# Optimization experiments

Measured on AMD Instinct MI355X. Metric: run time of the kernel, lower is better.

## Reference

```python
import jax, jax.numpy as jnp
import numpy as np

B, N, S, C1, C2 = 8, 8192, 2048, 128, 256
IN_CH = C1 + C2
MLP = [256, 128]
EPS_INTERP = 1e-8
EPS_BN = 1e-5


def setup_inputs() -> dict:
    key = jax.random.key(0)
    ks = jax.random.split(key, 8)
    inp = {
        "xyz1": jax.random.normal(ks[0], (B, 3, N), dtype=jnp.float32),
        "xyz2": jax.random.normal(ks[1], (B, 3, S), dtype=jnp.float32),
        "points1": jax.random.normal(ks[2], (B, C1, N), dtype=jnp.float32),
        "points2": jax.random.normal(ks[3], (B, C2, S), dtype=jnp.float32),
        # Conv1d(k=1) weights as [out, in] matrices, plus BN gamma/beta
        "W1": jax.random.normal(ks[4], (MLP[0], IN_CH), dtype=jnp.float32) * 0.02,
        "b1": jnp.zeros((MLP[0],), dtype=jnp.float32),
        "g1": jnp.ones((MLP[0],), dtype=jnp.float32),
        "be1": jnp.zeros((MLP[0],), dtype=jnp.float32),
        "W2": jax.random.normal(ks[5], (MLP[1], MLP[0]), dtype=jnp.float32) * 0.02,
        "b2": jnp.zeros((MLP[1],), dtype=jnp.float32),
        "g2": jnp.ones((MLP[1],), dtype=jnp.float32),
        "be2": jnp.zeros((MLP[1],), dtype=jnp.float32),
    }
    return inp


def _conv_bn_relu(x, W, b, g, be):
    # x: [B, N, Cin]; 1x1 Conv1d == per-point matmul; BN over (batch, length) per channel (training-mode stats)
    y = jnp.einsum('bnc,oc->bno', x, W) + b
    m = jnp.mean(y, axis=(0, 1))
    v = jnp.var(y, axis=(0, 1))
    return jax.nn.relu((y - m) * jax.lax.rsqrt(v + EPS_BN) * g + be)


def reference(xyz1, xyz2, points1, points2, W1, b1, g1, be1, W2, b2, g2, be2):
    x1 = xyz1.transpose(0, 2, 1)   # [B, N, 3]
    x2 = xyz2.transpose(0, 2, 1)   # [B, S, 3]
    p2 = points2.transpose(0, 2, 1)  # [B, S, C2]
    p1 = points1.transpose(0, 2, 1)  # [B, N, C1]

    # squared pairwise distances [B, N, S]
    d = (jnp.sum(x1 * x1, axis=-1, keepdims=True)
         - 2.0 * jnp.einsum('bnd,bsd->bns', x1, x2)
         + jnp.sum(x2 * x2, axis=-1)[:, None, :])

    # 3 nearest neighbors (smallest distances)
    neg_d, idx = jax.lax.top_k(-d, 3)          # idx: [B, N, 3]
    d3 = -neg_d                                 # [B, N, 3]
    recip = 1.0 / (d3 + EPS_INTERP)
    w = recip / jnp.sum(recip, axis=-1, keepdims=True)  # [B, N, 3]

    gathered = jax.vmap(lambda p, i: p[i])(p2, idx)     # [B, N, 3, C2]
    interp = jnp.sum(gathered * w[..., None], axis=2)   # [B, N, C2]

    x = jnp.concatenate([p1, interp], axis=-1)          # [B, N, C1+C2]
    x = _conv_bn_relu(x, W1, b1, g1, be1)
    x = _conv_bn_relu(x, W2, b2, g2, be2)
    return x.transpose(0, 2, 1)                         # [B, mlp[-1], N]
```

## Files before the change

### kernel.cpp

```cpp
#include <hip/hip_runtime.h>
#include <stdint.h>

#define B_ 8
#define N_ 8192
#define S_ 2048
#define C1_ 128
#define C2_ 256
#define IN_ 384
#define H1_ 256
#define H2_ 128
#define M_ (B_*N_)

typedef short bf16x8 __attribute__((ext_vector_type(8)));
typedef float f32x4 __attribute__((ext_vector_type(4)));

__device__ __forceinline__ float bf2f(unsigned short s){
  union { unsigned int u; float f; } x; x.u = ((unsigned int)s) << 16; return x.f;
}
__device__ __forceinline__ unsigned short f2bf(float f){
  union { float f; unsigned int u; } x; x.f = f;
  unsigned int u = x.u;
  unsigned int r = (u + 0x7FFFu + ((u >> 16) & 1u)) >> 16;
  return (unsigned short)r;
}

__device__ __forceinline__ size_t fragaddr(int m, int k, int K){
  return ((size_t)((m >> 4) * (K >> 5) + (k >> 5)) << 9)
       + (size_t)((((k >> 3) & 3) << 7) + ((m & 15) << 3) + (k & 7));
}

__device__ __forceinline__ void gload_lds16(const unsigned short* g, unsigned short* l){
  __builtin_amdgcn_global_load_lds(
      (const __attribute__((address_space(1))) unsigned int*)g,
      (__attribute__((address_space(3))) unsigned int*)l, 16, 0, 0);
}

__global__ __launch_bounds__(256) void prep_kernel(const float* W1, const float* W2,
                                                   unsigned short* w1b, unsigned short* w2b,
                                                   float* stats){
  int i = blockIdx.x * 256 + threadIdx.x;
  if (i < 256*384){
    int row = i / 384, col = i - row*384;
    w1b[fragaddr(row, col, 384)] = f2bf(W1[i]);
  }
  if (i < 128*256){
    int row = i >> 8, col = i & 255;
    w2b[fragaddr(row, col, 256)] = f2bf(W2[i]);
  }
  if (i < 1536) stats[i] = 0.f;
}

__global__ __launch_bounds__(256) void transpose_kernel(const float* in, unsigned short* out,
                                                        int rows_in, int cols_in,
                                                        int out_stride, int out_col_off){
  __shared__ float tile[32][33];
  int b  = blockIdx.z;
  int l0 = blockIdx.x * 32, r0 = blockIdx.y * 32;
  int tx = threadIdx.x & 31, ty = threadIdx.x >> 5;
  const float* src = in + (size_t)b * rows_in * cols_in;
  #pragma unroll
  for (int rr = ty; rr < 32; rr += 8)
    tile[rr][tx] = src[(size_t)(r0 + rr) * cols_in + l0 + tx];
  __syncthreads();
  unsigned short* dst = out + (size_t)b * cols_in * out_stride;
  #pragma unroll
  for (int rr = ty; rr < 32; rr += 8)
    dst[(size_t)(l0 + rr) * out_stride + out_col_off + r0 + tx] = f2bf(tile[tx][rr]);
}

__global__ __launch_bounds__(256) void transpose_p1_frag_kernel(const float* in, unsigned short* x){
  __shared__ float tile[32][33];
  int b  = blockIdx.z;
  int l0 = blockIdx.x * 32, r0 = blockIdx.y * 32;
  int tx = threadIdx.x & 31, ty = threadIdx.x >> 5;
  const float* src = in + (size_t)b * C1_ * N_;
  #pragma unroll
  for (int rr = ty; rr < 32; rr += 8)
    tile[rr][tx] = src[(size_t)(r0 + rr) * N_ + l0 + tx];
  __syncthreads();
  #pragma unroll
  for (int rr = ty; rr < 32; rr += 8){
    int g = b * N_ + l0 + rr;
    size_t a = ((size_t)((g >> 4)*12 + (r0 >> 5)) << 9)
             + (size_t)((((tx >> 3) & 3) << 7) + ((g & 15) << 3) + (tx & 7));
    x[a] = f2bf(tile[tx][rr]);
  }
}

#define PIECES_ 8
#define SPP_ (S_ / PIECES_)

__device__ __forceinline__ void insert_k(float& k0, float& k1, float& k2, float x){
  k2 = __builtin_amdgcn_fmed3f(k1, k2, x);
  k1 = __builtin_amdgcn_fmed3f(k0, k1, x);
  k0 = fminf(k0, x);
}

__device__ __forceinline__ void insert3(float& d0, float& d1, float& d2,
                                        int& i0, int& i1, int& i2,
                                        float x, int s){
  bool b0 = x < d0, b1 = x < d1, b2 = x < d2;
  i2 = b1 ? i1 : (b2 ? s : i2);
  i1 = b0 ? i0 : (b1 ? s : i1);
  i0 = b0 ? s : i0;
  d2 = __builtin_amdgcn_fmed3f(d1, d2, x);
  d1 = __builtin_amdgcn_fmed3f(d0, d1, x);
  d0 = fminf(d0, x);
}

__global__ __launch_bounds__(256, 8) void knn_kernel(const float* xyz1, const float* xyz2,
                                                     float* partd, int* parti){
  __shared__ float4 pts[SPP_];
  int b = blockIdx.y, piece = blockIdx.z;
  int n = blockIdx.x * 256 + threadIdx.x;
  int base = piece * SPP_;
  const float* x2 = xyz2 + (size_t)b * 3 * S_;
  {
    int i = threadIdx.x;
    float px = x2[base + i], py = x2[S_ + base + i], pz = x2[2*S_ + base + i];
    pts[i] = make_float4(-2.f*px, -2.f*py, -2.f*pz, px*px + py*py + pz*pz);
  }
  __syncthreads();
  const float* x1 = xyz1 + (size_t)b * 3 * N_;
  float ax = x1[n], ay = x1[N_ + n], az = x1[2*N_ + n];
  float x1sq = ax*ax + ay*ay + az*az;

  const float KINIT = __uint_as_float(0x7F000000u);
  float k[2][3];
  k[0][0]=k[0][1]=k[0][2]=KINIT;
  k[1][0]=k[1][1]=k[1][2]=KINIT;

  for (int s = 0; s < SPP_; s += 8){
    #pragma unroll
    for (int u = 0; u < 8; u++){
      float4 c = pts[s + u];
      float dd = fmaf(ax, c.x, fmaf(ay, c.y, fmaf(az, c.z, c.w + x1sq)));
      dd = fmaxf(dd, 0.f);
      float key = __uint_as_float((__float_as_uint(dd) & 0xFFFFFF00u) | (unsigned)(s + u));
      int L = u & 1;
      insert_k(k[L][0], k[L][1], k[L][2], key);
    }
  }
  float e0 = k[0][0], e1 = k[0][1], e2 = k[0][2];
  insert_k(e0, e1, e2, k[1][0]);
  insert_k(e0, e1, e2, k[1][1]);
  insert_k(e0, e1, e2, k[1][2]);

  float ed[3]; int ei[3];
  float ev[3] = {e0, e1, e2};
  #pragma unroll
  for (int j = 0; j < 3; j++){
    int li = (int)(__float_as_uint(ev[j]) & 0xFFu);
    float4 c = pts[li];
    float dd = fmaf(ax, c.x, fmaf(ay, c.y, fmaf(az, c.z, c.w + x1sq)));
    ed[j] = fmaxf(dd, 0.f);
    ei[j] = base + li;
  }

  size_t g = (size_t)b * N_ + n;
  partd[(piece*3 + 0)*(size_t)M_ + g] = ed[0];
  partd[(piece*3 + 1)*(size_t)M_ + g] = ed[1];
  partd[(piece*3 + 2)*(size_t)M_ + g] = ed[2];
  parti[(piece*3 + 0)*(size_t)M_ + g] = ei[0];
  parti[(piece*3 + 1)*(size_t)M_ + g] = ei[1];
  parti[(piece*3 + 2)*(size_t)M_ + g] = ei[2];
}

__global__ __launch_bounds__(256) void knn_merge_kernel(const float* partd, const int* parti,
                                                        int* idx, float* wgt){
  size_t g = (size_t)blockIdx.x * 256 + threadIdx.x;
  float d0 = partd[0*(size_t)M_ + g], d1 = partd[1*(size_t)M_ + g], d2 = partd[2*(size_t)M_ + g];
  int   i0 = parti[0*(size_t)M_ + g], i1 = parti[1*(size_t)M_ + g], i2 = parti[2*(size_t)M_ + g];
  #pragma unroll
  for (int p = 1; p < PIECES_; p++)
    #pragma unroll
    for (int j = 0; j < 3; j++)
      insert3(d0, d1, d2, i0, i1, i2,
              partd[(p*3 + j)*(size_t)M_ + g], parti[(p*3 + j)*(size_t)M_ + g]);

  float r0 = 1.f/(d0 + 1e-8f), r1 = 1.f/(d1 + 1e-8f), r2 = 1.f/(d2 + 1e-8f);
  float rs = 1.f/(r0 + r1 + r2);
  idx[g*3+0] = i0; idx[g*3+1] = i1; idx[g*3+2] = i2;
  wgt[g*3+0] = r0*rs; wgt[g*3+1] = r1*rs; wgt[g*3+2] = r2*rs;
}

__global__ __launch_bounds__(256) void interp_kernel(const int* idx, const float* wgt,
                                                     const unsigned short* p2t, unsigned short* x){
  int t = threadIdx.x;
  int base = blockIdx.x * 16;
  size_t suboff = (size_t)((((t >> 3) & 3) << 7) + (t & 7));
  for (int k = 0; k < 16; k++){
    int g = base + k;
    int b = g >> 13;
    const int*   ip = idx + (size_t)g * 3;
    const float* wp = wgt + (size_t)g * 3;
    const unsigned short* p = p2t + (size_t)b * S_ * C2_;
    float v = wp[0]*bf2f(p[(size_t)ip[0]*C2_ + t])
            + wp[1]*bf2f(p[(size_t)ip[1]*C2_ + t])
            + wp[2]*bf2f(p[(size_t)ip[2]*C2_ + t]);
    size_t a = ((size_t)((g >> 4)*12 + 4 + (t >> 5)) << 9) + suboff + (size_t)((g & 15) << 3);
    x[a] = f2bf(v);
  }
}

__device__ __forceinline__ bf16x8 bn_relu_frag(bf16x8 v, const float* a, const float* c, int kb){
  union { bf16x8 h; unsigned short s[8]; } u; u.h = v;
  union { float4 v4; float f[4]; } a0, a1, c0, c1;
  a0.v4 = *(const float4*)(a + kb);  a1.v4 = *(const float4*)(a + kb + 4);
  c0.v4 = *(const float4*)(c + kb);  c1.v4 = *(const float4*)(c + kb + 4);
  #pragma unroll
  for (int j = 0; j < 4; j++){
    float f0 = fmaf(a0.f[j], bf2f(u.s[j]),     c0.f[j]);
    float f1 = fmaf(a1.f[j], bf2f(u.s[j + 4]), c1.f[j]);
    u.s[j]     = f2bf(fmaxf(f0, 0.f));
    u.s[j + 4] = f2bf(fmaxf(f1, 0.f));
  }
  return u.h;
}

template<int K, bool HAS_AFF, bool OUT_FRAG>
__global__ __launch_bounds__(256) void gemm_lds_kernel(
    const unsigned short* __restrict__ A, const unsigned short* __restrict__ Wf,
    unsigned short* __restrict__ Cout, int Ntot,
    float* sumv, float* sqv, const float* aff_a, const float* aff_c)
{
  constexpr int KT = K / 32;
  __shared__ unsigned short smA[128*32];
  __shared__ unsigned short smB[128*32];
  __shared__ float ldsStat[256];

  const int t = threadIdx.x;
  const int lane = t & 63, wave = t >> 6;
  const int ln = lane & 15, lq = lane >> 4;
  const int wm = wave >> 1, wn = wave & 1;
  const int mtb = blockIdx.x * 8;
  const int ntb = blockIdx.y * 8;
  const int mtw = mtb + wm * 4;
  const int n0  = blockIdx.y * 128 + wn * 64;

  ldsStat[t] = 0.f;

  const int c0 = 2*wave, c1 = 2*wave + 1;
  const unsigned short* gA0 = A  + (((size_t)((mtb + c0)*KT)) << 9) + lane*8;
  const unsigned short* gA1 = A  + (((size_t)((mtb + c1)*KT)) << 9) + lane*8;
  const unsigned short* gB0 = Wf + (((size_t)((ntb + c0)*KT)) << 9) + lane*8;
  const unsigned short* gB1 = Wf + (((size_t)((ntb + c1)*KT)) << 9) + lane*8;
  unsigned short* lA0 = &smA[(c0 << 9) + lane*8];
  unsigned short* lA1 = &smA[(c1 << 9) + lane*8];
  unsigned short* lB0 = &smB[(c0 << 9) + lane*8];
  unsigned short* lB1 = &smB[(c1 << 9) + lane*8];

  const f32x4 fzero = {0.f, 0.f, 0.f, 0.f};
  f32x4 acc[4][4];
  #pragma unroll
  for (int i = 0; i < 4; i++)
    #pragma unroll
    for (int j = 0; j < 4; j++) acc[i][j] = fzero;

  for (int kt = 0; kt < KT; kt++){
    const size_t koff = (size_t)kt << 9;
    gload_lds16(gA0 + koff, lA0);
    gload_lds16(gA1 + koff, lA1);
    gload_lds16(gB0 + koff, lB0);
    gload_lds16(gB1 + koff, lB1);
    __syncthreads();

    bf16x8 af[4], bf[4];
    #pragma unroll
    for (int i = 0; i < 4; i++)
      af[i] = *(const bf16x8*)(&smA[((wm*4 + i) << 9) + lane*8]);
    #pragma unroll
    for (int j = 0; j < 4; j++)
      bf[j] = *(const bf16x8*)(&smB[((wn*4 + j) << 9) + lane*8]);
    if (HAS_AFF){
      const int kb = kt*32 + lq*8;
      #pragma unroll
      for (int i = 0; i < 4; i++) af[i] = bn_relu_frag(af[i], aff_a, aff_c, kb);
    }
    #pragma unroll
    for (int i = 0; i < 4; i++)
      #pragma unroll
      for (int j = 0; j < 4; j++)
        acc[i][j] = __builtin_amdgcn_mfma_f32_16x16x32_bf16(af[i], bf[j], acc[i][j], 0, 0, 0);
    __syncthreads();
  }

  #pragma unroll
  for (int j = 0; j < 4; j++){
    int ncol = n0 + j*16 + ln;
    float s = 0.f, q = 0.f;
    #pragma unroll
    for (int i = 0; i < 4; i++){
      #pragma unroll
      for (int r = 0; r < 4; r++){
        float v = acc[i][j][r];
        if (OUT_FRAG){
          size_t a = ((size_t)((mtw + i)*8 + (ncol >> 5)) << 9)
                   + (size_t)((((ncol >> 3) & 3) << 7) + ((lq*4 + r) << 3) + (ncol & 7));
          Cout[a] = f2bf(v);
        } else {
          Cout[((size_t)((mtw + i)*16 + lq*4 + r)) * Ntot + ncol] = f2bf(v);
        }
        s += v; q += v*v;
      }
    }
    s += __shfl_xor(s, 16); s += __shfl_xor(s, 32);
    q += __shfl_xor(q, 16); q += __shfl_xor(q, 32);
    if (lq == 0){
      int colLocal = wn*64 + j*16 + ln;
      atomicAdd(&ldsStat[colLocal], s);
      atomicAdd(&ldsStat[128 + colLocal], q);
    }
  }
  __syncthreads();
  {
    float v = ldsStat[t];
    int col = blockIdx.y*128 + (t & 127);
    atomicAdd((t < 128 ? &sumv[col] : &sqv[col]), v);
  }
}

__global__ void finalize_kernel(const float* sum, const float* sq, const float* g, const float* be,
                                float* a_out, float* c_out, int C){
  int c = threadIdx.x;
  if (c < C){
    float mean = sum[c] * (1.f / M_);
    float var  = sq[c]  * (1.f / M_) - mean*mean;
    float a = g[c] * rsqrtf(var + 1e-5f);
    a_out[c] = a;
    c_out[c] = fmaf(-mean, a, be[c]);
  }
}

__global__ __launch_bounds__(256) void out_kernel(const unsigned short* y2, const float* a2,
                                                  const float* c2, float* out){
  __shared__ float lds[64][65];
  int t  = threadIdx.x;
  int b  = blockIdx.z;
  int n0 = blockIdx.y * 64;
  int c0 = blockIdx.x * 64;
  int cc = t & 63, tr = t >> 6;
  float a = a2[c0 + cc], cadd = c2[c0 + cc];
  #pragma unroll
  for (int ph = 0; ph < 16; ph++){
    int nr = tr + ph*4;
    unsigned short v = y2[((size_t)(b*N_ + n0 + nr)) * H2_ + c0 + cc];
    lds[nr][cc] = fmaxf(fmaf(a, bf2f(v), cadd), 0.f);
  }
  __syncthreads();
  #pragma unroll
  for (int ph = 0; ph < 16; ph++){
    int cr = tr + ph*4;
    out[((size_t)(b*H2_ + c0 + cr)) * N_ + n0 + cc] = lds[cc][cr];
  }
}

extern "C" void kernel_launch(void* const* d_in, const int* in_sizes, int n_in,
                              void* d_out, int out_size, void* d_ws, size_t ws_size,
                              hipStream_t stream){
  const float* xyz1 = (const float*)d_in[0];
  const float* xyz2 = (const float*)d_in[1];
  const float* p1   = (const float*)d_in[2];
  const float* p2   = (const float*)d_in[3];
  const float* W1   = (const float*)d_in[4];
  const float* g1   = (const float*)d_in[6];
  const float* be1  = (const float*)d_in[7];
  const float* W2   = (const float*)d_in[8];
  const float* g2   = (const float*)d_in[10];
  const float* be2  = (const float*)d_in[11];
  float* out = (float*)d_out;

  char* ws = (char*)d_ws;
  unsigned short* x    = (unsigned short*)(ws + 0);
  unsigned short* p2t  = (unsigned short*)(ws + 50331648);
  unsigned short* y1   = (unsigned short*)(ws + 58720256);
  unsigned short* y2   = (unsigned short*)(ws + 92274688);
  unsigned short* w1b  = (unsigned short*)(ws + 109051904);
  unsigned short* w2b  = (unsigned short*)(ws + 109248512);
  int*            idx  = (int*)(ws + 109314048);
  float*          wgt  = (float*)(ws + 110100480);
  float*          stats= (float*)(ws + 110886912);
  float* sum1 = stats;        float* sq1 = stats + 256;
  float* sum2 = stats + 512;  float* sq2 = stats + 640;
  float* a1   = stats + 768;  float* c1  = stats + 1024;
  float* a2   = stats + 1280; float* c2  = stats + 1408;
  float* partd = (float*)y1;
  int*   parti = (int*)(y1 + 6291456);

  prep_kernel<<<384, 256, 0, stream>>>(W1, W2, w1b, w2b, stats);
  transpose_kernel<<<dim3(64, 8, 8), 256, 0, stream>>>(p2, p2t, 256, 2048, 256, 0);
  transpose_p1_frag_kernel<<<dim3(256, 4, 8), 256, 0, stream>>>(p1, x);
  knn_kernel<<<dim3(32, 8, PIECES_), 256, 0, stream>>>(xyz1, xyz2, partd, parti);
  knn_merge_kernel<<<256, 256, 0, stream>>>(partd, parti, idx, wgt);
  interp_kernel<<<4096, 256, 0, stream>>>(idx, wgt, p2t, x);
  gemm_lds_kernel<384, false, true><<<dim3(512, 2), 256, 0, stream>>>(
      x, w1b, y1, 256, sum1, sq1, nullptr, nullptr);
  finalize_kernel<<<1, 256, 0, stream>>>(sum1, sq1, g1, be1, a1, c1, 256);
  gemm_lds_kernel<256, true, false><<<dim3(512, 1), 256, 0, stream>>>(
      y1, w2b, y2, 128, sum2, sq2, a1, c1);
  finalize_kernel<<<1, 256, 0, stream>>>(sum2, sq2, g2, be2, a2, c2, 128);
  out_kernel<<<dim3(2, 128, 8), 256, 0, stream>>>(y2, a2, c2, out);
}
```

Baseline: 270.3 us.

## Fuse prep/transpose kernels, merge KNN into interp, double K-step per GEMM sync

Three prep kernels (weight conversion, p2 transpose, p1 fragment transpose) are combined into one launch that dispatches on block index. The KNN merge is folded into the interpolation kernel, so 16 threads per block merge the partial top-3 lists into shared memory and the idx/wgt round trip through global memory disappears. The GEMM now loads two 32-wide K slices per barrier pair, which halves the number of __syncthreads but doubles the LDS tiles. In exchange, the merge runs on only 16 threads per block while the rest wait, and larger LDS use may lower occupancy.

```diff
diff --git a/kernel.cpp b/kernel.cpp
--- a/kernel.cpp
+++ b/kernel.cpp
@@ -35,55 +35,58 @@
       (__attribute__((address_space(3))) unsigned int*)l, 16, 0, 0);
 }
 
-__global__ __launch_bounds__(256) void prep_kernel(const float* W1, const float* W2,
-                                                   unsigned short* w1b, unsigned short* w2b,
-                                                   float* stats){
-  int i = blockIdx.x * 256 + threadIdx.x;
-  if (i < 256*384){
-    int row = i / 384, col = i - row*384;
-    w1b[fragaddr(row, col, 384)] = f2bf(W1[i]);
-  }
-  if (i < 128*256){
-    int row = i >> 8, col = i & 255;
-    w2b[fragaddr(row, col, 256)] = f2bf(W2[i]);
-  }
-  if (i < 1536) stats[i] = 0.f;
-}
-
-__global__ __launch_bounds__(256) void transpose_kernel(const float* in, unsigned short* out,
-                                                        int rows_in, int cols_in,
-                                                        int out_stride, int out_col_off){
+__global__ __launch_bounds__(256) void prep_fused_kernel(const float* W1, const float* W2,
+                                                         const float* p2, const float* p1,
+                                                         unsigned short* w1b, unsigned short* w2b,
+                                                         float* stats, unsigned short* p2t,
+                                                         unsigned short* x){
   __shared__ float tile[32][33];
-  int b  = blockIdx.z;
-  int l0 = blockIdx.x * 32, r0 = blockIdx.y * 32;
+  int bx = blockIdx.x;
+  if (bx < 384){
+    int i = bx * 256 + threadIdx.x;
+    if (i < 256*384){
+      int row = i / 384, col = i - row*384;
+      w1b[fragaddr(row, col, 384)] = f2bf(W1[i]);
+    }
+    if (i < 128*256){
+      int row = i >> 8, col = i & 255;
+      w2b[fragaddr(row, col, 256)] = f2bf(W2[i]);
+    }
+    if (i < 1536) stats[i] = 0.f;
+    return;
+  }
   int tx = threadIdx.x & 31, ty = threadIdx.x >> 5;
-  const float* src = in + (size_t)b * rows_in * cols_in;
-  #pragma unroll
-  for (int rr = ty; rr < 32; rr += 8)
-    tile[rr][tx] = src[(size_t)(r0 + rr) * cols_in + l0 + tx];
-  __syncthreads();
-  unsigned short* dst = out + (size_t)b * cols_in * out_stride;
-  #pragma unroll
-  for (int rr = ty; rr < 32; rr += 8)
-    dst[(size_t)(l0 + rr) * out_stride + out_col_off + r0 + tx] = f2bf(tile[tx][rr]);
-}
-
-__global__ __launch_bounds__(256) void transpose_p1_frag_kernel(const float* in, unsigned short* x){
-  __shared__ float tile[32][33];
-  int b  = blockIdx.z;
-  int l0 = blockIdx.x * 32, r0 = blockIdx.y * 32;
-  int tx = threadIdx.x & 31, ty = threadIdx.x >> 5;
-  const float* src = in + (size_t)b * C1_ * N_;
-  #pragma unroll
-  for (int rr = ty; rr < 32; rr += 8)
-    tile[rr][tx] = src[(size_t)(r0 + rr) * N_ + l0 + tx];
-  __syncthreads();
-  #pragma unroll
-  for (int rr = ty; rr < 32; rr += 8){
-    int g = b * N_ + l0 + rr;
-    size_t a = ((size_t)((g >> 4)*12 + (r0 >> 5)) << 9)
-             + (size_t)((((tx >> 3) & 3) << 7) + ((g & 15) << 3) + (tx & 7));
-    x[a] = f2bf(tile[tx][rr]);
+  if (bx < 4480){
+    int id = bx - 384;
+    int b = id >> 9, rem = id & 511;
+    int l0 = (rem & 63) * 32, r0 = (rem >> 6) * 32;
+    const float* src = p2 + (size_t)b * C2_ * S_;
+    #pragma unroll
+    for (int rr = ty; rr < 32; rr += 8)
+      tile[rr][tx] = src[(size_t)(r0 + rr) * S_ + l0 + tx];
+    __syncthreads();
+    unsigned short* dst = p2t + (size_t)b * S_ * C2_;
+    #pragma unroll
+    for (int rr = ty; rr < 32; rr += 8)
+      dst[(size_t)(l0 + rr) * C2_ + r0 + tx] = f2bf(tile[tx][rr]);
+    return;
+  }
+  {
+    int id = bx - 4480;
+    int b = id >> 10, rem = id & 1023;
+    int l0 = (rem & 255) * 32, r0 = (rem >> 8) * 32;
+    const float* src = p1 + (size_t)b * C1_ * N_;
+    #pragma unroll
+    for (int rr = ty; rr < 32; rr += 8)
+      tile[rr][tx] = src[(size_t)(r0 + rr) * N_ + l0 + tx];
+    __syncthreads();
+    #pragma unroll
+    for (int rr = ty; rr < 32; rr += 8){
+      int g = b * N_ + l0 + rr;
+      size_t a = ((size_t)((g >> 4)*12 + (r0 >> 5)) << 9)
+               + (size_t)((((tx >> 3) & 3) << 7) + ((g & 15) << 3) + (tx & 7));
+      x[a] = f2bf(tile[tx][rr]);
+    }
   }
 }
 
@@ -166,38 +169,36 @@
   parti[(piece*3 + 2)*(size_t)M_ + g] = ei[2];
 }
 
-__global__ __launch_bounds__(256) void knn_merge_kernel(const float* partd, const int* parti,
-                                                        int* idx, float* wgt){
-  size_t g = (size_t)blockIdx.x * 256 + threadIdx.x;
-  float d0 = partd[0*(size_t)M_ + g], d1 = partd[1*(size_t)M_ + g], d2 = partd[2*(size_t)M_ + g];
-  int   i0 = parti[0*(size_t)M_ + g], i1 = parti[1*(size_t)M_ + g], i2 = parti[2*(size_t)M_ + g];
-  #pragma unroll
-  for (int p = 1; p < PIECES_; p++)
-    #pragma unroll
-    for (int j = 0; j < 3; j++)
-      insert3(d0, d1, d2, i0, i1, i2,
-              partd[(p*3 + j)*(size_t)M_ + g], parti[(p*3 + j)*(size_t)M_ + g]);
-
-  float r0 = 1.f/(d0 + 1e-8f), r1 = 1.f/(d1 + 1e-8f), r2 = 1.f/(d2 + 1e-8f);
-  float rs = 1.f/(r0 + r1 + r2);
-  idx[g*3+0] = i0; idx[g*3+1] = i1; idx[g*3+2] = i2;
-  wgt[g*3+0] = r0*rs; wgt[g*3+1] = r1*rs; wgt[g*3+2] = r2*rs;
-}
-
-__global__ __launch_bounds__(256) void interp_kernel(const int* idx, const float* wgt,
+__global__ __launch_bounds__(256) void interp_kernel(const float* partd, const int* parti,
                                                      const unsigned short* p2t, unsigned short* x){
+  __shared__ int   sidx[16][3];
+  __shared__ float swgt[16][3];
   int t = threadIdx.x;
   int base = blockIdx.x * 16;
+  if (t < 16){
+    size_t g = (size_t)base + t;
+    float d0 = partd[0*(size_t)M_ + g], d1 = partd[1*(size_t)M_ + g], d2 = partd[2*(size_t)M_ + g];
+    int   i0 = parti[0*(size_t)M_ + g], i1 = parti[1*(size_t)M_ + g], i2 = parti[2*(size_t)M_ + g];
+    #pragma unroll
+    for (int p = 1; p < PIECES_; p++)
+      #pragma unroll
+      for (int j = 0; j < 3; j++)
+        insert3(d0, d1, d2, i0, i1, i2,
+                partd[(p*3 + j)*(size_t)M_ + g], parti[(p*3 + j)*(size_t)M_ + g]);
+    float r0 = 1.f/(d0 + 1e-8f), r1 = 1.f/(d1 + 1e-8f), r2 = 1.f/(d2 + 1e-8f);
+    float rs = 1.f/(r0 + r1 + r2);
+    sidx[t][0] = i0; sidx[t][1] = i1; sidx[t][2] = i2;
+    swgt[t][0] = r0*rs; swgt[t][1] = r1*rs; swgt[t][2] = r2*rs;
+  }
+  __syncthreads();
   size_t suboff = (size_t)((((t >> 3) & 3) << 7) + (t & 7));
   for (int k = 0; k < 16; k++){
     int g = base + k;
     int b = g >> 13;
-    const int*   ip = idx + (size_t)g * 3;
-    const float* wp = wgt + (size_t)g * 3;
     const unsigned short* p = p2t + (size_t)b * S_ * C2_;
-    float v = wp[0]*bf2f(p[(size_t)ip[0]*C2_ + t])
-            + wp[1]*bf2f(p[(size_t)ip[1]*C2_ + t])
-            + wp[2]*bf2f(p[(size_t)ip[2]*C2_ + t]);
+    float v = swgt[k][0]*bf2f(p[(size_t)sidx[k][0]*C2_ + t])
+            + swgt[k][1]*bf2f(p[(size_t)sidx[k][1]*C2_ + t])
+            + swgt[k][2]*bf2f(p[(size_t)sidx[k][2]*C2_ + t]);
     size_t a = ((size_t)((g >> 4)*12 + 4 + (t >> 5)) << 9) + suboff + (size_t)((g & 15) << 3);
     x[a] = f2bf(v);
   }
@@ -225,8 +226,8 @@
     float* sumv, float* sqv, const float* aff_a, const float* aff_c)
 {
   constexpr int KT = K / 32;
-  __shared__ unsigned short smA[128*32];
-  __shared__ unsigned short smB[128*32];
+  __shared__ unsigned short smA[128*64];
+  __shared__ unsigned short smB[128*64];
   __shared__ float ldsStat[256];
 
   const int t = threadIdx.x;
@@ -241,14 +242,6 @@
   ldsStat[t] = 0.f;
 
   const int c0 = 2*wave, c1 = 2*wave + 1;
-  const unsigned short* gA0 = A  + (((size_t)((mtb + c0)*KT)) << 9) + lane*8;
-  const unsigned short* gA1 = A  + (((size_t)((mtb + c1)*KT)) << 9) + lane*8;
-  const unsigned short* gB0 = Wf + (((size_t)((ntb + c0)*KT)) << 9) + lane*8;
-  const unsigned short* gB1 = Wf + (((size_t)((ntb + c1)*KT)) << 9) + lane*8;
-  unsigned short* lA0 = &smA[(c0 << 9) + lane*8];
-  unsigned short* lA1 = &smA[(c1 << 9) + lane*8];
-  unsigned short* lB0 = &smB[(c0 << 9) + lane*8];
-  unsigned short* lB1 = &smB[(c1 << 9) + lane*8];
 
   const f32x4 fzero = {0.f, 0.f, 0.f, 0.f};
   f32x4 acc[4][4];
@@ -257,31 +250,39 @@
     #pragma unroll
     for (int j = 0; j < 4; j++) acc[i][j] = fzero;
 
-  for (int kt = 0; kt < KT; kt++){
-    const size_t koff = (size_t)kt << 9;
-    gload_lds16(gA0 + koff, lA0);
-    gload_lds16(gA1 + koff, lA1);
-    gload_lds16(gB0 + koff, lB0);
-    gload_lds16(gB1 + koff, lB1);
+  for (int kk = 0; kk < KT; kk += 2){
+    #pragma unroll
+    for (int q = 0; q < 2; q++){
+      gload_lds16(A  + (((size_t)((mtb + c0)*KT + kk + q)) << 9) + lane*8,
+                  &smA[((c0*2 + q) << 9) + lane*8]);
+      gload_lds16(A  + (((size_t)((mtb + c1)*KT + kk + q)) << 9) + lane*8,
+                  &smA[((c1*2 + q) << 9) + lane*8]);
+      gload_lds16(Wf + (((size_t)((ntb + c0)*KT + kk + q)) << 9) + lane*8,
+                  &smB[((c0*2 + q) << 9) + lane*8]);
+      gload_lds16(Wf + (((size_t)((ntb + c1)*KT + kk + q)) << 9) + lane*8,
+                  &smB[((c1*2 + q) << 9) + lane*8]);
+    }
     __syncthreads();
-
-    bf16x8 af[4], bf[4];
-    #pragma unroll
-    for (int i = 0; i < 4; i++)
-      af[i] = *(const bf16x8*)(&smA[((wm*4 + i) << 9) + lane*8]);
-    #pragma unroll
-    for (int j = 0; j < 4; j++)
-      bf[j] = *(const bf16x8*)(&smB[((wn*4 + j) << 9) + lane*8]);
-    if (HAS_AFF){
-      const int kb = kt*32 + lq*8;
-      #pragma unroll
-      for (int i = 0; i < 4; i++) af[i] = bn_relu_frag(af[i], aff_a, aff_c, kb);
-    }
-    #pragma unroll
-    for (int i = 0; i < 4; i++)
+    #pragma unroll
+    for (int q = 0; q < 2; q++){
+      bf16x8 af[4], bf[4];
+      #pragma unroll
+      for (int i = 0; i < 4; i++)
+        af[i] = *(const bf16x8*)(&smA[(((wm*4 + i)*2 + q) << 9) + lane*8]);
       #pragma unroll
       for (int j = 0; j < 4; j++)
-        acc[i][j] = __builtin_amdgcn_mfma_f32_16x16x32_bf16(af[i], bf[j], acc[i][j], 0, 0, 0);
+        bf[j] = *(const bf16x8*)(&smB[(((wn*4 + j)*2 + q) << 9) + lane*8]);
+      if (HAS_AFF){
+        const int kb = (kk + q)*32 + lq*8;
+        #pragma unroll
+        for (int i = 0; i < 4; i++) af[i] = bn_relu_frag(af[i], aff_a, aff_c, kb);
+      }
+      #pragma unroll
+      for (int i = 0; i < 4; i++)
+        #pragma unroll
+        for (int j = 0; j < 4; j++)
+          acc[i][j] = __builtin_amdgcn_mfma_f32_16x16x32_bf16(af[i], bf[j], acc[i][j], 0, 0, 0);
+    }
     __syncthreads();
   }
 
@@ -377,8 +378,6 @@
   unsigned short* y2   = (unsigned short*)(ws + 92274688);
   unsigned short* w1b  = (unsigned short*)(ws + 109051904);
   unsigned short* w2b  = (unsigned short*)(ws + 109248512);
-  int*            idx  = (int*)(ws + 109314048);
-  float*          wgt  = (float*)(ws + 110100480);
   float*          stats= (float*)(ws + 110886912);
   float* sum1 = stats;        float* sq1 = stats + 256;
   float* sum2 = stats + 512;  float* sq2 = stats + 640;
@@ -387,12 +386,9 @@
   float* partd = (float*)y1;
   int*   parti = (int*)(y1 + 6291456);
 
-  prep_kernel<<<384, 256, 0, stream>>>(W1, W2, w1b, w2b, stats);
-  transpose_kernel<<<dim3(64, 8, 8), 256, 0, stream>>>(p2, p2t, 256, 2048, 256, 0);
-  transpose_p1_frag_kernel<<<dim3(256, 4, 8), 256, 0, stream>>>(p1, x);
+  prep_fused_kernel<<<12672, 256, 0, stream>>>(W1, W2, p2, p1, w1b, w2b, stats, p2t, x);
   knn_kernel<<<dim3(32, 8, PIECES_), 256, 0, stream>>>(xyz1, xyz2, partd, parti);
-  knn_merge_kernel<<<256, 256, 0, stream>>>(partd, parti, idx, wgt);
-  interp_kernel<<<4096, 256, 0, stream>>>(idx, wgt, p2t, x);
+  interp_kernel<<<4096, 256, 0, stream>>>(partd, parti, p2t, x);
   gemm_lds_kernel<384, false, true><<<dim3(512, 2), 256, 0, stream>>>(
       x, w1b, y1, 256, sum1, sq1, nullptr, nullptr);
   finalize_kernel<<<1, 256, 0, stream>>>(sum1, sq1, g1, be1, a1, c1, 256);
```

New measurement: 267.7 us. About the same (-1.0%).
